# Kernel tuning notes

Hardware: AMD Instinct MI355X
Metric: run time of the kernel (lower is better)

## Reference

```python
import jax, jax.numpy as jnp
import numpy as np

DIM = 180
WS = 16        # window_size
OWS = 24       # overlap_win_size = int(16*0.5)+16
HEADS = 6
HD = DIM // HEADS
MLP_HID = DIM * 2
TABLE = (WS + OWS - 1) ** 2  # 1521
H = W = 256
B = 1


def layernorm(x, g, b, eps=1e-5):
    mu = x.mean(-1, keepdims=True)
    d = x - mu
    var = (d * d).mean(-1, keepdims=True)
    return g * d / jnp.sqrt(var + eps) + b


def setup_inputs() -> dict:
    key = jax.random.key(0)
    ks = jax.random.split(key, 12)
    std = 0.02
    inp = {
        'x': jax.random.normal(ks[0], (B, H * W, DIM), jnp.float32),
        'rpi': jax.random.randint(ks[1], (WS * WS, OWS * OWS), 0, TABLE, jnp.int32),
        'h': H,
        'w': W,
        'norm1_g': jnp.ones((DIM,), jnp.float32),
        'norm1_b': jnp.zeros((DIM,), jnp.float32),
        'q_w': jax.random.normal(ks[2], (DIM, DIM), jnp.float32) * std,
        'q_b': jnp.zeros((DIM,), jnp.float32),
        'kv_w': jax.random.normal(ks[3], (DIM, 2 * DIM), jnp.float32) * std,
        'kv_b': jnp.zeros((2 * DIM,), jnp.float32),
        'rpb_table': jax.random.normal(ks[4], (TABLE, HEADS), jnp.float32) * std,
        'proj_w': jax.random.normal(ks[5], (DIM, DIM), jnp.float32) * std,
        'proj_b': jnp.zeros((DIM,), jnp.float32),
        'norm2_g': jnp.ones((DIM,), jnp.float32),
        'norm2_b': jnp.zeros((DIM,), jnp.float32),
        'mlp_w1': jax.random.normal(ks[6], (DIM, MLP_HID), jnp.float32) * std,
        'mlp_b1': jnp.zeros((MLP_HID,), jnp.float32),
        'mlp_w2': jax.random.normal(ks[7], (MLP_HID, DIM), jnp.float32) * std,
        'mlp_b2': jnp.zeros((DIM,), jnp.float32),
    }
    return inp


def reference(x, rpi, h, w, norm1_g, norm1_b, q_w, q_b, kv_w, kv_b,
              rpb_table, proj_w, proj_b, norm2_g, norm2_b,
              mlp_w1, mlp_b1, mlp_w2, mlp_b2):
    b, L, c = x.shape
    ws, ows, heads = WS, OWS, HEADS
    d = c // heads
    scale = d ** -0.5
    pad = (ows - ws) // 2  # 4
    nh, nw = h // ws, w // ws
    nq, n = ws * ws, ows * ows
    b_ = b * nh * nw

    shortcut = x
    xn = layernorm(x, norm1_g, norm1_b)
    x_img = xn.reshape(b, h, w, c)

    q = x_img @ q_w + q_b                    # [b,h,w,c]
    kv = x_img @ kv_w + kv_b                 # [b,h,w,2c] (k | v)

    # window_partition for q -> [b_, nq, c]
    qw = q.reshape(b, nh, ws, nw, ws, c).transpose(0, 1, 3, 2, 4, 5)
    qw = qw.reshape(b_, nq, c)

    # nn.Unfold(kernel=ows, stride=ws, padding=pad) on kv -> overlapping windows
    kvp = jnp.pad(kv, ((0, 0), (pad, pad), (pad, pad), (0, 0)))
    rows = (jnp.arange(nh) * ws)[:, None] + jnp.arange(ows)   # [nh, ows]
    cols = (jnp.arange(nw) * ws)[:, None] + jnp.arange(ows)   # [nw, ows]
    t = kvp[:, rows]                         # [b, nh, ows, W+2p, 2c]
    t = t[:, :, :, cols]                     # [b, nh, ows, nw, ows, 2c]
    t = t.transpose(0, 1, 3, 2, 4, 5).reshape(b_, n, 2 * c)
    k_win, v_win = t[..., :c], t[..., c:]

    qh = qw.reshape(b_, nq, heads, d).transpose(0, 2, 1, 3) * scale
    kh = k_win.reshape(b_, n, heads, d).transpose(0, 2, 1, 3)
    vh = v_win.reshape(b_, n, heads, d).transpose(0, 2, 1, 3)

    attn = jnp.einsum('bhqd,bhkd->bhqk', qh, kh)              # [b_,heads,nq,n]
    bias = rpb_table[rpi.reshape(-1)].reshape(nq, n, heads).transpose(2, 0, 1)
    attn = jax.nn.softmax(attn + bias[None], axis=-1)
    out = jnp.einsum('bhqk,bhkd->bhqd', attn, vh)
    out = out.transpose(0, 2, 1, 3).reshape(b_, nq, c)

    # window_reverse -> [b, h*w, c]
    xo = out.reshape(b, nh, nw, ws, ws, c).transpose(0, 1, 3, 2, 4, 5)
    xo = xo.reshape(b, h * w, c)

    xo = xo @ proj_w + proj_b + shortcut
    xn2 = layernorm(xo, norm2_g, norm2_b)
    mlp = jax.nn.gelu(xn2 @ mlp_w1 + mlp_b1, approximate=False) @ mlp_w2 + mlp_b2
    return xo + mlp
```

## Files before the change

### kernel.cpp

```cpp
#include <hip/hip_runtime.h>
#include <hip/hip_bf16.h>
#include <stdint.h>

#define DIM 180
#define WS 16
#define OWS 24
#define HEADS 6
#define HD 30
#define MLP_HID 360
#define HH 256
#define WW 256
#define L (HH * WW)
#define NWIN 256
#define NQ 256
#define NK 576

#define KP1 192
#define KP2 384
#define NQKV 576

#define QSCALE 0.2633988734672831f
#define LOG2E 1.4426950408889634f

typedef float f4v __attribute__((ext_vector_type(4)));
typedef short s8v __attribute__((ext_vector_type(8)));
typedef short s4v __attribute__((ext_vector_type(4)));

static __device__ __forceinline__ short f2bf(float x) {
    union { __hip_bfloat16 h; short s; } u;
    u.h = __float2bfloat16(x);
    return u.s;
}
static __device__ __forceinline__ uint32_t pack_bf2(float lo, float hi) {
    union { __hip_bfloat162 h; uint32_t u; } u;
    u.h.x = __float2bfloat16(lo);
    u.h.y = __float2bfloat16(hi);
    return u.u;
}
static __device__ __forceinline__ float bflo(uint32_t u) {
    union { uint32_t i; float f; } c; c.i = u << 16; return c.f;
}
static __device__ __forceinline__ float bfhi(uint32_t u) {
    union { uint32_t i; float f; } c; c.i = u & 0xffff0000u; return c.f;
}

typedef __attribute__((address_space(1))) const unsigned int ga_u32;
typedef __attribute__((address_space(3))) unsigned int la_u32;
static __device__ __forceinline__ void gld16(const void* g, void* l) {
    __builtin_amdgcn_global_load_lds((ga_u32*)g, (la_u32*)l, 16, 0, 0);
}

__global__ __launch_bounds__(64) void ln_kernel(const float* __restrict__ x,
                                                const float* __restrict__ g,
                                                const float* __restrict__ b,
                                                __hip_bfloat16* __restrict__ out) {
    int row = blockIdx.x;
    int t = threadIdx.x;
    const float* xr = x + (size_t)row * DIM;
    float v0 = xr[t];
    float v1 = xr[t + 64];
    float v2 = (t < DIM - 128) ? xr[t + 128] : 0.f;
    float s = v0 + v1 + v2;
    #pragma unroll
    for (int o = 32; o > 0; o >>= 1) s += __shfl_down(s, o);
    s = __shfl(s, 0);
    float mu = s * (1.f / DIM);
    float d0 = v0 - mu, d1 = v1 - mu;
    float d2 = (t < DIM - 128) ? (v2 - mu) : 0.f;
    float vs = d0 * d0 + d1 * d1 + d2 * d2;
    #pragma unroll
    for (int o = 32; o > 0; o >>= 1) vs += __shfl_down(vs, o);
    vs = __shfl(vs, 0);
    float rstd = rsqrtf(vs * (1.f / DIM) + 1e-5f);
    __hip_bfloat16* orow = out + (size_t)row * KP1;
    orow[t]      = __float2bfloat16(g[t] * d0 * rstd + b[t]);
    orow[t + 64] = __float2bfloat16(g[t + 64] * d1 * rstd + b[t + 64]);
    if (t < DIM - 128)
        orow[t + 128] = __float2bfloat16(g[t + 128] * d2 * rstd + b[t + 128]);
    if (t < KP1 - DIM) orow[DIM + t] = __float2bfloat16(0.f);
}

__global__ __launch_bounds__(256) void bias_kernel(const int* __restrict__ rpi,
                                                   const float* __restrict__ rpb,
                                                   ushort* __restrict__ biasC) {
    int idx = blockIdx.x * 256 + threadIdx.x;
    int j = idx & 15;
    int q = (idx >> 4) & 255;
    int r = idx >> 12;
    int kc = r % 36;
    int head = r / 36;
    int k = (kc >> 1) * 32 + ((j >> 2) << 3) + ((kc & 1) << 2) + (j & 3);
    int t = rpi[q * NK + k];
    biasC[idx] = (ushort)f2bf(rpb[t * HEADS + head] * LOG2E);
}

__global__ __launch_bounds__(256) void wconv_kernel(
        const float* __restrict__ qw, const float* __restrict__ kvw,
        const float* __restrict__ pw, const float* __restrict__ w1,
        const float* __restrict__ w2, short* __restrict__ wt) {
    int idx = blockIdx.x * 256 + threadIdx.x;
    float v = 0.f;
    if (idx < 110592) {
        int n = idx / KP1, k = idx - n * KP1;
        if (k < DIM) {
            if (n < DIM) v = qw[k * DIM + n] * QSCALE;
            else if (n < 540) v = kvw[k * (2 * DIM) + (n - DIM)];
        }
    } else if (idx < 147456) {
        int r = idx - 110592;
        int n = r / KP1, k = r - n * KP1;
        if (k < DIM && n < DIM) v = pw[k * DIM + n];
    } else if (idx < 221184) {
        int r = idx - 147456;
        int n = r / KP1, k = r - n * KP1;
        if (k < DIM && n < MLP_HID) v = w1[k * MLP_HID + n];
    } else {
        int r = idx - 221184;
        int n = r / KP2, k = r - n * KP2;
        if (k < MLP_HID && n < DIM) v = w2[k * DIM + n];
    }
    wt[idx] = f2bf(v);
}

__global__ __launch_bounds__(256) void bconv_kernel(
        const float* __restrict__ qb, const float* __restrict__ kvb,
        const float* __restrict__ pb, const float* __restrict__ b1,
        const float* __restrict__ b2, float* __restrict__ bv) {
    int idx = blockIdx.x * 256 + threadIdx.x;
    if (idx >= 1344) return;
    float v = 0.f;
    if (idx < 576) {
        if (idx < DIM) v = qb[idx] * QSCALE;
        else if (idx < 540) v = kvb[idx - DIM];
    } else if (idx < 768) {
        int n = idx - 576; if (n < DIM) v = pb[n];
    } else if (idx < 1152) {
        int n = idx - 768; if (n < MLP_HID) v = b1[n];
    } else {
        int n = idx - 1152; if (n < DIM) v = b2[n];
    }
    bv[idx] = v;
}

__global__ __launch_bounds__(256) void mgemm(
        const short* __restrict__ A, const short* __restrict__ Wt,
        const float* __restrict__ bias,
        float* __restrict__ outf, short* __restrict__ outb,
        int lda, int ldo, int nK, int mode) {
    __shared__ short As[2][128 * 32];
    __shared__ short Wsm[2][64 * 32];
    int tid = threadIdx.x;
    int lane = tid & 63, wave = tid >> 6;
    int q15 = lane & 15, quad = lane >> 4;
    int n0 = blockIdx.x * 64;
    int m0 = blockIdx.y * 128;

    auto stage = [&](int buf, int k0) {
        int lr = lane >> 2, c = lane & 3;
        const short* Ab = A + (size_t)m0 * lda + k0;
        #pragma unroll
        for (int i = 0; i < 2; i++) {
            int r = i * 64 + wave * 16 + lr;
            gld16(Ab + (size_t)r * lda + ((c ^ (r & 3)) * 8),
                  &As[buf][(i * 64 + wave * 16) * 32]);
        }
        const short* Wb = Wt + (size_t)n0 * lda + k0;
        {
            int r = wave * 16 + lr;
            gld16(Wb + (size_t)r * lda + ((c ^ (r & 3)) * 8),
                  &Wsm[buf][(wave * 16) * 32]);
        }
    };

    f4v acc[2][4];
    #pragma unroll
    for (int a = 0; a < 2; a++)
        #pragma unroll
        for (int b = 0; b < 4; b++) acc[a][b] = (f4v){0.f, 0.f, 0.f, 0.f};

    stage(0, 0);
    __syncthreads();
    for (int ch = 0; ch < nK; ch++) {
        int buf = ch & 1;
        if (ch + 1 < nK) stage(buf ^ 1, (ch + 1) * 32);
        s8v af[2], wf[4];
        #pragma unroll
        for (int mt = 0; mt < 2; mt++) {
            int r = wave * 32 + mt * 16 + q15;
            af[mt] = *(const s8v*)&As[buf][r * 32 + ((quad ^ (r & 3)) * 8)];
        }
        #pragma unroll
        for (int nt = 0; nt < 4; nt++) {
            int r = nt * 16 + q15;
            wf[nt] = *(const s8v*)&Wsm[buf][r * 32 + ((quad ^ (r & 3)) * 8)];
        }
        #pragma unroll
        for (int mt = 0; mt < 2; mt++)
            #pragma unroll
            for (int nt = 0; nt < 4; nt++)
                acc[mt][nt] = __builtin_amdgcn_mfma_f32_16x16x32_bf16(
                    af[mt], wf[nt], acc[mt][nt], 0, 0, 0);
        __syncthreads();
    }

    #pragma unroll
    for (int mt = 0; mt < 2; mt++) {
        int mb = m0 + wave * 32 + mt * 16 + quad * 4;
        #pragma unroll
        for (int nt = 0; nt < 4; nt++) {
            int n = n0 + nt * 16 + q15;
            float bv = bias[n];
            f4v a = acc[mt][nt];
            #pragma unroll
            for (int r = 0; r < 4; r++) {
                int m = mb + r;
                float v = a[r] + bv;
                if (mode == 0) {
                    outb[(size_t)m * ldo + n] = f2bf(v);
                } else if (mode == 1) {
                    float ge = 0.5f * v * (1.f + erff(v * 0.70710678118654752f));
                    outb[(size_t)m * ldo + n] = f2bf(ge);
                } else {
                    if (n < DIM) outf[(size_t)m * DIM + n] += v;
                }
            }
        }
    }
}

__global__ __launch_bounds__(256) void projln(
        const short* __restrict__ A, const short* __restrict__ Wt,
        const float* __restrict__ bias, const float* __restrict__ resid,
        const float* __restrict__ g2, const float* __restrict__ b2,
        float* __restrict__ outf, short* __restrict__ outb) {
    __shared__ short As[2][64 * 32];
    __shared__ short Wsm[2][192 * 32];
    int tid = threadIdx.x;
    int lane = tid & 63, wave = tid >> 6;
    int q15 = lane & 15, quad = lane >> 4;
    int m0 = blockIdx.x * 64;

    auto stage = [&](int buf, int k0) {
        int lr = lane >> 2, c = lane & 3;
        const short* Ab = A + (size_t)m0 * KP1 + k0;
        {
            int r = wave * 16 + lr;
            gld16(Ab + (size_t)r * KP1 + ((c ^ (r & 3)) * 8),
                  &As[buf][(wave * 16) * 32]);
        }
        #pragma unroll
        for (int i = 0; i < 3; i++) {
            int r = i * 64 + wave * 16 + lr;
            gld16(Wt + (size_t)r * KP1 + k0 + ((c ^ (r & 3)) * 8),
                  &Wsm[buf][(i * 64 + wave * 16) * 32]);
        }
    };

    f4v acc[12];
    #pragma unroll
    for (int b = 0; b < 12; b++) acc[b] = (f4v){0.f, 0.f, 0.f, 0.f};

    stage(0, 0);
    __syncthreads();
    for (int ch = 0; ch < KP1 / 32; ch++) {
        int buf = ch & 1;
        if (ch + 1 < KP1 / 32) stage(buf ^ 1, (ch + 1) * 32);
        int ra = wave * 16 + q15;
        s8v af = *(const s8v*)&As[buf][ra * 32 + ((quad ^ (ra & 3)) * 8)];
        #pragma unroll
        for (int nt = 0; nt < 12; nt++) {
            int r = nt * 16 + q15;
            s8v wf = *(const s8v*)&Wsm[buf][r * 32 + ((quad ^ (r & 3)) * 8)];
            acc[nt] = __builtin_amdgcn_mfma_f32_16x16x32_bf16(af, wf, acc[nt], 0, 0, 0);
        }
        __syncthreads();
    }

    float gv[12], bv[12], biasv[12];
    #pragma unroll
    for (int nt = 0; nt < 12; nt++) {
        int n = nt * 16 + q15;
        biasv[nt] = bias[n];
        gv[nt] = (n < DIM) ? g2[n] : 0.f;
        bv[nt] = (n < DIM) ? b2[n] : 0.f;
    }
    int mb = m0 + wave * 16 + quad * 4;
    #pragma unroll
    for (int r = 0; r < 4; r++) {
        int m = mb + r;
        float v[12];
        float s = 0.f, ss = 0.f;
        #pragma unroll
        for (int nt = 0; nt < 12; nt++) {
            int n = nt * 16 + q15;
            float x = acc[nt][r] + biasv[nt];
            if (n < DIM) x += resid[(size_t)m * DIM + n];
            else x = 0.f;
            v[nt] = x;
            s += x;
            ss += x * x;
        }
        #pragma unroll
        for (int o = 8; o > 0; o >>= 1) {
            s += __shfl_xor(s, o);
            ss += __shfl_xor(ss, o);
        }
        float mu = s * (1.f / DIM);
        float var = ss * (1.f / DIM) - mu * mu;
        float rstd = rsqrtf(var + 1e-5f);
        #pragma unroll
        for (int nt = 0; nt < 12; nt++) {
            int n = nt * 16 + q15;
            if (n < DIM) outf[(size_t)m * DIM + n] = v[nt];
            outb[(size_t)m * KP1 + n] = f2bf(gv[nt] * (v[nt] - mu) * rstd + bv[nt]);
        }
    }
}

#define CHUNK 32
#define NCHUNK (NK / CHUNK)

__global__ __launch_bounds__(512) void attn_kernel(
        const __hip_bfloat16* __restrict__ qkvb,
        const ushort* __restrict__ biasC, __hip_bfloat16* __restrict__ aout) {
    __shared__ __align__(16) short Ks[2][CHUNK][32];
    __shared__ __align__(16) short Vt[2][32][40];

    int tid = threadIdx.x;
    int lane = tid & 63;
    int wave = tid >> 6;
    int q15 = lane & 15;
    int quad = lane >> 4;
    int bid = blockIdx.x;
    int grp = bid / 48;
    int r48 = bid - grp * 48;
    int head = r48 >> 3;
    int win = grp * 8 + (r48 & 7);
    int bh = win >> 4, bw = win & 15;

    const uint32_t* kvd = (const uint32_t*)qkvb;

    s8v qf[2];
    #pragma unroll
    for (int qt = 0; qt < 2; qt++) {
        int q = wave * 32 + qt * 16 + q15;
        int qy = q >> 4, qx = q & 15;
        size_t pos = (size_t)(bh * WS + qy) * WW + (bw * WS + qx);
        const uint32_t* qp = kvd + pos * 288 + head * 15 + quad * 4;
        uint32_t w0 = qp[0], w1 = qp[1], w2 = qp[2], w3 = qp[3];
        union { uint32_t u[4]; s8v v; } cv;
        cv.u[0] = w0; cv.u[1] = w1; cv.u[2] = w2; cv.u[3] = w3;
        qf[qt] = cv.v;
    }
    if (head == 0 && tid < 256) {
        int qy = tid >> 4, qx = tid & 15;
        size_t pos = (size_t)(bh * WS + qy) * WW + (bw * WS + qx);
        uint2 z = make_uint2(0u, 0u);
        uint2* oz = (uint2*)(aout + pos * KP1 + DIM);
        oz[0] = z; oz[1] = z; oz[2] = z;
    }

    bool lowh = tid < 256;
    int t2 = lowh ? tid : tid - 256;
    int keyK = t2 >> 3, pK = t2 & 7;
    int keyV = t2 & 31, pp = t2 >> 5;
    int pKs = pK ^ (((keyK >> 3) & 3) << 1);

    auto rowbase = [&](int jk) -> const uint32_t* {
        int oy = jk / OWS, ox = jk - oy * OWS;
        int y = bh * WS - 4 + oy, x = bw * WS - 4 + ox;
        if ((unsigned)y < HH && (unsigned)x < WW)
            return kvd + ((size_t)y * WW + x) * 288;
        return nullptr;
    };
    auto loadKV = [&](int c0, uint32_t& a, uint32_t& b) {
        a = b = 0u;
        if (lowh) {
            const uint32_t* rk = rowbase(c0 + keyK);
            if (rk) {
                const uint32_t* kp = rk + 90 + head * 15 + pK * 2;
                a = kp[0];
                if (pK < 7) b = kp[1];
            }
        } else {
            const uint32_t* rv = rowbase(c0 + keyV);
            if (rv) {
                const uint32_t* vp = rv + 180 + head * 15 + pp * 2;
                a = vp[0];
                if (pp < 7) b = vp[1];
            }
        }
    };
    auto writeKV = [&](int bufi, uint32_t a, uint32_t b) {
        if (lowh) {
            *(uint2*)&Ks[bufi][keyK][pKs * 4] = make_uint2(a, b);
        } else {
            int d0 = pp * 4;
            Vt[bufi][d0][keyV]     = (short)(a & 0xffff);
            Vt[bufi][d0 + 1][keyV] = (short)(a >> 16);
            if (pp < 7) {
                Vt[bufi][d0 + 2][keyV] = (short)(b & 0xffff);
                Vt[bufi][d0 + 3][keyV] = (short)(b >> 16);
            } else {
                Vt[bufi][30][keyV] = (short)0x3F80;
                Vt[bufi][31][keyV] = 0;
            }
        }
    };

    const char* bBase = (const char*)biasC +
        ((size_t)head * (36 * 256 * 16) + (size_t)(wave * 32 + q15) * 16 + quad * 4) * 2;
    uint2 bb[2][2];
    auto loadBias = [&](int ch) {
        #pragma unroll
        for (int kt = 0; kt < 2; kt++)
            #pragma unroll
            for (int qt = 0; qt < 2; qt++)
                bb[kt][qt] = *(const uint2*)(bBase + (size_t)(ch * 2 + kt) * 8192 + qt * 512);
    };

    uint32_t aA, bA, aB, bB2;

    loadKV(0, aA, bA);
    loadKV(CHUNK, aB, bB2);
    loadBias(0);
    writeKV(0, aA, bA);
    __syncthreads();

    f4v oacc[2][2];
    #pragma unroll
    for (int a = 0; a < 2; a++)
        #pragma unroll
        for (int b = 0; b < 2; b++) oacc[a][b] = (f4v){0.f, 0.f, 0.f, 0.f};

    int pr = ((q15 & 12) << 1) | (q15 & 3);
    int rslot = (quad ^ (q15 >> 2)) * 8;

    auto body = [&](int ch, int bufR,
                    uint32_t& aR, uint32_t& bR, uint32_t& aW, uint32_t& bW) {
        s8v kf0 = *(const s8v*)&Ks[bufR][pr][rslot];
        s8v kf1 = *(const s8v*)&Ks[bufR][pr + 4][rslot];
        s8v va0 = *(const s8v*)&Vt[bufR][q15][quad * 8];
        s8v va1 = *(const s8v*)&Vt[bufR][16 + q15][quad * 8];

        f4v zf = (f4v){0.f, 0.f, 0.f, 0.f};
        f4v s0[2], s1[2];
        #pragma unroll
        for (int qt = 0; qt < 2; qt++) {
            s0[qt] = __builtin_amdgcn_mfma_f32_16x16x32_bf16(kf0, qf[qt], zf, 0, 0, 0);
            s1[qt] = __builtin_amdgcn_mfma_f32_16x16x32_bf16(kf1, qf[qt], zf, 0, 0, 0);
        }
        if (ch + 2 < NCHUNK) loadKV((ch + 2) * CHUNK, aR, bR);

        s8v pbv[2];
        #pragma unroll
        for (int qt = 0; qt < 2; qt++) {
            uint2 b0 = bb[0][qt], b1 = bb[1][qt];
            union { uint32_t u[4]; s8v v; } pk;
            pk.u[0] = pack_bf2(__builtin_amdgcn_exp2f(s0[qt][0] + bflo(b0.x)),
                               __builtin_amdgcn_exp2f(s0[qt][1] + bfhi(b0.x)));
            pk.u[1] = pack_bf2(__builtin_amdgcn_exp2f(s0[qt][2] + bflo(b0.y)),
                               __builtin_amdgcn_exp2f(s0[qt][3] + bfhi(b0.y)));
            pk.u[2] = pack_bf2(__builtin_amdgcn_exp2f(s1[qt][0] + bflo(b1.x)),
                               __builtin_amdgcn_exp2f(s1[qt][1] + bfhi(b1.x)));
            pk.u[3] = pack_bf2(__builtin_amdgcn_exp2f(s1[qt][2] + bflo(b1.y)),
                               __builtin_amdgcn_exp2f(s1[qt][3] + bfhi(b1.y)));
            pbv[qt] = pk.v;
        }
        if (ch + 1 < NCHUNK) loadBias(ch + 1);

        #pragma unroll
        for (int qt = 0; qt < 2; qt++) {
            oacc[0][qt] = __builtin_amdgcn_mfma_f32_16x16x32_bf16(va0, pbv[qt], oacc[0][qt], 0, 0, 0);
            oacc[1][qt] = __builtin_amdgcn_mfma_f32_16x16x32_bf16(va1, pbv[qt], oacc[1][qt], 0, 0, 0);
        }

        if (ch + 1 < NCHUNK) writeKV(bufR ^ 1, aW, bW);

        asm volatile("s_waitcnt lgkmcnt(0)" ::: "memory");
        __builtin_amdgcn_sched_barrier(0);
        __builtin_amdgcn_s_barrier();
    };

    #pragma unroll 1
    for (int t = 0; t < NCHUNK / 2; t++) {
        body(2 * t,     0, aA, bA, aB, bB2);
        body(2 * t + 1, 1, aB, bB2, aA, bA);
    }

    #pragma unroll
    for (int qt = 0; qt < 2; qt++) {
        float l = __shfl(oacc[1][qt][2], 48 | q15);
        float rl = 1.0f / l;
        int q = wave * 32 + qt * 16 + q15;
        int qy = q >> 4, qx = q & 15;
        size_t pos = (size_t)(bh * WS + qy) * WW + (bw * WS + qx);
        uint32_t* od = (uint32_t*)(aout + pos * KP1 + head * HD);
        int dh = quad * 2;
        f4v o0 = oacc[0][qt], o1 = oacc[1][qt];
        od[dh]     = pack_bf2(o0[0] * rl, o0[1] * rl);
        od[dh + 1] = pack_bf2(o0[2] * rl, o0[3] * rl);
        od[8 + dh] = pack_bf2(o1[0] * rl, o1[1] * rl);
        if (quad < 3)
            od[8 + dh + 1] = pack_bf2(o1[2] * rl, o1[3] * rl);
    }
}

extern "C" void kernel_launch(void* const* d_in, const int* in_sizes, int n_in,
                              void* d_out, int out_size, void* d_ws, size_t ws_size,
                              hipStream_t stream) {
    const float* x      = (const float*)d_in[0];
    const int*   rpi    = (const int*)d_in[1];
    const float* n1g    = (const float*)d_in[4];
    const float* n1b    = (const float*)d_in[5];
    const float* q_w    = (const float*)d_in[6];
    const float* q_b    = (const float*)d_in[7];
    const float* kv_w   = (const float*)d_in[8];
    const float* kv_b   = (const float*)d_in[9];
    const float* rpb    = (const float*)d_in[10];
    const float* proj_w = (const float*)d_in[11];
    const float* proj_b = (const float*)d_in[12];
    const float* n2g    = (const float*)d_in[13];
    const float* n2b    = (const float*)d_in[14];
    const float* w1     = (const float*)d_in[15];
    const float* b1     = (const float*)d_in[16];
    const float* w2     = (const float*)d_in[17];
    const float* b2     = (const float*)d_in[18];
    float* out = (float*)d_out;

    char* ws = (char*)d_ws;
    short* qkvb  = (short*)(ws);
    short* xn    = (short*)(ws + 75497472ull);
    ushort* biasC = (ushort*)(ws + 100663296ull);
    short* wt    = (short*)(ws + 104202240ull);
    short* wt_qkv  = wt;
    short* wt_proj = wt + 110592;
    short* wt_1    = wt + 147456;
    short* wt_2    = wt + 221184;
    float* bvec  = (float*)(ws + 104202240ull + 589824ull);
    float* b_qkv  = bvec;
    float* b_proj = bvec + 576;
    float* b_1    = bvec + 768;
    float* b_2    = bvec + 1152;
    short* ao  = xn;
    short* xn2 = qkvb;
    short* h1  = qkvb + 12582912;

    bias_kernel<<<884736 / 256, 256, 0, stream>>>(rpi, rpb, biasC);
    wconv_kernel<<<294912 / 256, 256, 0, stream>>>(q_w, kv_w, proj_w, w1, w2, wt);
    bconv_kernel<<<6, 256, 0, stream>>>(q_b, kv_b, proj_b, b1, b2, bvec);
    ln_kernel<<<L, 64, 0, stream>>>(x, n1g, n1b, (__hip_bfloat16*)xn);
    mgemm<<<dim3(NQKV / 64, L / 128), 256, 0, stream>>>(
        xn, wt_qkv, b_qkv, nullptr, qkvb, KP1, NQKV, KP1 / 32, 0);
    attn_kernel<<<NWIN * HEADS, 512, 0, stream>>>(
        (const __hip_bfloat16*)qkvb, biasC, (__hip_bfloat16*)ao);
    projln<<<L / 64, 256, 0, stream>>>(
        ao, wt_proj, b_proj, x, n2g, n2b, out, xn2);
    mgemm<<<dim3(KP2 / 64, L / 128), 256, 0, stream>>>(
        xn2, wt_1, b_1, nullptr, h1, KP1, KP2, KP1 / 32, 1);
    mgemm<<<dim3(KP1 / 64, L / 128), 256, 0, stream>>>(
        h1, wt_2, b_2, out, nullptr, KP2, 0, KP2 / 32, 3);
}
```

Before: 396.7 us.

## Widen GEMM N-tile to 192, batch LayerNorm rows, use tanh GELU

The bf16 MFMA GEMM now computes 128x192 output tiles instead of 128x64, so each staged A tile is reused across three times as many columns and there are fewer blocks and redundant A loads. LayerNorm processes four rows per 256-thread block instead of one row per 64-thread block. The MLP GELU switches from exact erf to a tanh approximation computed with exp2, which slightly changes numerics. Larger accumulator arrays raise register pressure and may reduce occupancy.

After: 411.0 us. 1.04x slower.

```diff
diff --git a/kernel.cpp b/kernel.cpp
--- a/kernel.cpp
+++ b/kernel.cpp
@@ -50,12 +50,12 @@
     __builtin_amdgcn_global_load_lds((ga_u32*)g, (la_u32*)l, 16, 0, 0);
 }
 
-__global__ __launch_bounds__(64) void ln_kernel(const float* __restrict__ x,
-                                                const float* __restrict__ g,
-                                                const float* __restrict__ b,
-                                                __hip_bfloat16* __restrict__ out) {
-    int row = blockIdx.x;
-    int t = threadIdx.x;
+__global__ __launch_bounds__(256) void ln_kernel(const float* __restrict__ x,
+                                                 const float* __restrict__ g,
+                                                 const float* __restrict__ b,
+                                                 __hip_bfloat16* __restrict__ out) {
+    int row = blockIdx.x * 4 + (threadIdx.x >> 6);
+    int t = threadIdx.x & 63;
     const float* xr = x + (size_t)row * DIM;
     float v0 = xr[t];
     float v1 = xr[t + 64];
@@ -142,17 +142,17 @@
     bv[idx] = v;
 }
 
-__global__ __launch_bounds__(256) void mgemm(
+__global__ __launch_bounds__(256) void mgemm192(
         const short* __restrict__ A, const short* __restrict__ Wt,
         const float* __restrict__ bias,
         float* __restrict__ outf, short* __restrict__ outb,
         int lda, int ldo, int nK, int mode) {
     __shared__ short As[2][128 * 32];
-    __shared__ short Wsm[2][64 * 32];
+    __shared__ short Wsm[2][192 * 32];
     int tid = threadIdx.x;
     int lane = tid & 63, wave = tid >> 6;
     int q15 = lane & 15, quad = lane >> 4;
-    int n0 = blockIdx.x * 64;
+    int n0 = blockIdx.x * 192;
     int m0 = blockIdx.y * 128;
 
     auto stage = [&](int buf, int k0) {
@@ -164,42 +164,38 @@
             gld16(Ab + (size_t)r * lda + ((c ^ (r & 3)) * 8),
                   &As[buf][(i * 64 + wave * 16) * 32]);
         }
-        const short* Wb = Wt + (size_t)n0 * lda + k0;
-        {
-            int r = wave * 16 + lr;
-            gld16(Wb + (size_t)r * lda + ((c ^ (r & 3)) * 8),
-                  &Wsm[buf][(wave * 16) * 32]);
-        }
-    };
-
-    f4v acc[2][4];
+        #pragma unroll
+        for (int i = 0; i < 3; i++) {
+            int r = i * 64 + wave * 16 + lr;
+            gld16(Wt + (size_t)(n0 + r) * lda + k0 + ((c ^ (r & 3)) * 8),
+                  &Wsm[buf][(i * 64 + wave * 16) * 32]);
+        }
+    };
+
+    f4v acc[2][12];
     #pragma unroll
     for (int a = 0; a < 2; a++)
         #pragma unroll
-        for (int b = 0; b < 4; b++) acc[a][b] = (f4v){0.f, 0.f, 0.f, 0.f};
+        for (int b = 0; b < 12; b++) acc[a][b] = (f4v){0.f, 0.f, 0.f, 0.f};
 
     stage(0, 0);
     __syncthreads();
     for (int ch = 0; ch < nK; ch++) {
         int buf = ch & 1;
         if (ch + 1 < nK) stage(buf ^ 1, (ch + 1) * 32);
-        s8v af[2], wf[4];
+        s8v af[2];
         #pragma unroll
         for (int mt = 0; mt < 2; mt++) {
             int r = wave * 32 + mt * 16 + q15;
             af[mt] = *(const s8v*)&As[buf][r * 32 + ((quad ^ (r & 3)) * 8)];
         }
         #pragma unroll
-        for (int nt = 0; nt < 4; nt++) {
+        for (int nt = 0; nt < 12; nt++) {
             int r = nt * 16 + q15;
-            wf[nt] = *(const s8v*)&Wsm[buf][r * 32 + ((quad ^ (r & 3)) * 8)];
-        }
-        #pragma unroll
-        for (int mt = 0; mt < 2; mt++)
-            #pragma unroll
-            for (int nt = 0; nt < 4; nt++)
-                acc[mt][nt] = __builtin_amdgcn_mfma_f32_16x16x32_bf16(
-                    af[mt], wf[nt], acc[mt][nt], 0, 0, 0);
+            s8v wf = *(const s8v*)&Wsm[buf][r * 32 + ((quad ^ (r & 3)) * 8)];
+            acc[0][nt] = __builtin_amdgcn_mfma_f32_16x16x32_bf16(af[0], wf, acc[0][nt], 0, 0, 0);
+            acc[1][nt] = __builtin_amdgcn_mfma_f32_16x16x32_bf16(af[1], wf, acc[1][nt], 0, 0, 0);
+        }
         __syncthreads();
     }
 
@@ -207,7 +203,7 @@
     for (int mt = 0; mt < 2; mt++) {
         int mb = m0 + wave * 32 + mt * 16 + quad * 4;
         #pragma unroll
-        for (int nt = 0; nt < 4; nt++) {
+        for (int nt = 0; nt < 12; nt++) {
             int n = n0 + nt * 16 + q15;
             float bv = bias[n];
             f4v a = acc[mt][nt];
@@ -218,8 +214,10 @@
                 if (mode == 0) {
                     outb[(size_t)m * ldo + n] = f2bf(v);
                 } else if (mode == 1) {
-                    float ge = 0.5f * v * (1.f + erff(v * 0.70710678118654752f));
-                    outb[(size_t)m * ldo + n] = f2bf(ge);
+                    float y = 0.7978845608028654f * (v + 0.044715f * v * v * v);
+                    float e = __builtin_amdgcn_exp2f(y * 2.885390081777927f);
+                    float th = 1.f - 2.f / (1.f + e);
+                    outb[(size_t)m * ldo + n] = f2bf(0.5f * v * (1.f + th));
                 } else {
                     if (n < DIM) outf[(size_t)m * DIM + n] += v;
                 }
@@ -549,15 +547,15 @@
     bias_kernel<<<884736 / 256, 256, 0, stream>>>(rpi, rpb, biasC);
     wconv_kernel<<<294912 / 256, 256, 0, stream>>>(q_w, kv_w, proj_w, w1, w2, wt);
     bconv_kernel<<<6, 256, 0, stream>>>(q_b, kv_b, proj_b, b1, b2, bvec);
-    ln_kernel<<<L, 64, 0, stream>>>(x, n1g, n1b, (__hip_bfloat16*)xn);
-    mgemm<<<dim3(NQKV / 64, L / 128), 256, 0, stream>>>(
+    ln_kernel<<<L / 4, 256, 0, stream>>>(x, n1g, n1b, (__hip_bfloat16*)xn);
+    mgemm192<<<dim3(NQKV / 192, L / 128), 256, 0, stream>>>(
         xn, wt_qkv, b_qkv, nullptr, qkvb, KP1, NQKV, KP1 / 32, 0);
     attn_kernel<<<NWIN * HEADS, 512, 0, stream>>>(
         (const __hip_bfloat16*)qkvb, biasC, (__hip_bfloat16*)ao);
     projln<<<L / 64, 256, 0, stream>>>(
         ao, wt_proj, b_proj, x, n2g, n2b, out, xn2);
-    mgemm<<<dim3(KP2 / 64, L / 128), 256, 0, stream>>>(
+    mgemm192<<<dim3(KP2 / 192, L / 128), 256, 0, stream>>>(
         xn2, wt_1, b_1, nullptr, h1, KP1, KP2, KP1 / 32, 1);
-    mgemm<<<dim3(KP1 / 64, L / 128), 256, 0, stream>>>(
+    mgemm192<<<dim3(KP1 / 192, L / 128), 256, 0, stream>>>(
         h1, wt_2, b_2, out, nullptr, KP2, 0, KP2 / 32, 3);
 }
```
